# Performance work log

Hardware: AMD Instinct MI355X
Metric: run time of the kernel (lower is better)

Reference implementation:

```python
import jax, jax.numpy as jnp
import numpy as np

N_NODES = 100000
IN_DIM = 128
HIDDEN = 256
N_CLASSES = 16
N_EDGES = 1600000
N_GRAPHS = 64


def setup_inputs() -> dict:
    key = jax.random.key(0)
    ks = jax.random.split(key, 12)
    x = jax.random.normal(ks[0], (N_NODES, IN_DIM), dtype=jnp.float32)
    edge_index = jax.random.randint(ks[1], (2, N_EDGES), 0, N_NODES, dtype=jnp.int64)
    batch = jnp.sort(jax.random.randint(ks[2], (N_NODES,), 0, N_GRAPHS, dtype=jnp.int64))
    s = 0.05
    # SAGEConv layer 1: lin_l (on aggregated neighbors, with bias), lin_r (on root, no bias)
    W1l = jax.random.normal(ks[3], (IN_DIM, HIDDEN), dtype=jnp.float32) * s
    b1 = jnp.zeros((HIDDEN,), dtype=jnp.float32)
    W1r = jax.random.normal(ks[4], (IN_DIM, HIDDEN), dtype=jnp.float32) * s
    # SAGEConv layer 2
    W2l = jax.random.normal(ks[5], (HIDDEN, HIDDEN), dtype=jnp.float32) * s
    b2 = jnp.zeros((HIDDEN,), dtype=jnp.float32)
    W2r = jax.random.normal(ks[6], (HIDDEN, HIDDEN), dtype=jnp.float32) * s
    # final classifier
    fcW = jax.random.normal(ks[7], (HIDDEN, N_CLASSES), dtype=jnp.float32) * s
    fcb = jnp.zeros((N_CLASSES,), dtype=jnp.float32)
    return {"x": x, "edge_index": edge_index, "batch": batch,
            "W1l": W1l, "b1": b1, "W1r": W1r,
            "W2l": W2l, "b2": b2, "W2r": W2r,
            "fcW": fcW, "fcb": fcb}


def _sage_conv(x, src, dst, Wl, bl, Wr, n_nodes):
    # mean aggregation of neighbor features onto destination nodes
    agg = jax.ops.segment_sum(x[src], dst, num_segments=n_nodes)      # [N, d]
    deg = jax.ops.segment_sum(jnp.ones(src.shape, x.dtype), dst, num_segments=n_nodes)
    mean = agg / jnp.maximum(deg, 1.0)[:, None]
    # out = lin_l(mean_neighbors) + lin_r(x_root)  (PyG SAGEConv, mean aggr)
    return mean @ Wl + bl + x @ Wr


def reference(x, edge_index, batch, W1l, b1, W1r, W2l, b2, W2r, fcW, fcb):
    src, dst = edge_index[0], edge_index[1]
    h = jax.nn.relu(_sage_conv(x, src, dst, W1l, b1, W1r, N_NODES))
    # dropout is identity in inference mode
    h = jax.nn.relu(_sage_conv(h, src, dst, W2l, b2, W2r, N_NODES))
    # global mean pool over graphs in the batch
    g_sum = jax.ops.segment_sum(h, batch, num_segments=N_GRAPHS)      # [G, d]
    g_cnt = jax.ops.segment_sum(jnp.ones(batch.shape, h.dtype), batch, num_segments=N_GRAPHS)
    g = g_sum / jnp.maximum(g_cnt, 1.0)[:, None]
    return g @ fcW + fcb                                              # [G, num_classes]
```

## Files before the change

kernel.cpp:

```cpp
#include <hip/hip_runtime.h>

#define INDIM 128
#define HID 256
#define NCLS 16
#define NGRAPH 64
#define CHUNK 8192

typedef __bf16 bf16_t;
typedef bf16_t bf16x8 __attribute__((ext_vector_type(8)));
typedef float f32x4 __attribute__((ext_vector_type(4)));

__device__ __forceinline__ float bfu_lo(unsigned v) {
    union { unsigned i; float f; } u; u.i = v << 16; return u.f;
}
__device__ __forceinline__ float bfu_hi(unsigned v) {
    union { unsigned i; float f; } u; u.i = v & 0xffff0000u; return u.f;
}
__device__ __forceinline__ unsigned short f2bf(float f) {
    union { float f; unsigned i; } u; u.f = f;
    unsigned b = u.i;
    return (unsigned short)((b + 0x7fffu + ((b >> 16) & 1u)) >> 16);
}
__device__ __forceinline__ unsigned packbf(float lo, float hi) {
    return (unsigned)f2bf(lo) | ((unsigned)f2bf(hi) << 16);
}

typedef __attribute__((address_space(1))) const unsigned gu32_t;
typedef __attribute__((address_space(3))) unsigned lu32_t;
__device__ __forceinline__ void gl_lds16(const void* g, void* l) {
    __builtin_amdgcn_global_load_lds((gu32_t*)g, (lu32_t*)l, 16, 0, 0);
}

#define IACC(aE, aO, v)                              \
    do {                                             \
        aE[0] += ((v).x & 0x00FF00FFu);              \
        aO[0] += (((v).x >> 8) & 0x00FF00FFu);       \
        aE[1] += ((v).y & 0x00FF00FFu);              \
        aO[1] += (((v).y >> 8) & 0x00FF00FFu);       \
        aE[2] += ((v).z & 0x00FF00FFu);              \
        aO[2] += (((v).z >> 8) & 0x00FF00FFu);       \
        aE[3] += ((v).w & 0x00FF00FFu);              \
        aO[3] += (((v).w >> 8) & 0x00FF00FFu);       \
    } while (0)

__global__ void hist_kernel(const int* __restrict__ dst, int* __restrict__ deg, int E) {
    int e = blockIdx.x * blockDim.x + threadIdx.x;
    if (e < E) atomicAdd(&deg[dst[e]], 1);
}

__global__ void scan1_kernel(const int* __restrict__ deg, int* __restrict__ bsum, int n) {
    __shared__ int s[256];
    int t = threadIdx.x;
    int i = blockIdx.x * 256 + t;
    s[t] = (i < n) ? deg[i] : 0;
    __syncthreads();
    for (int off = 128; off > 0; off >>= 1) {
        if (t < off) s[t] += s[t + off];
        __syncthreads();
    }
    if (t == 0) bsum[blockIdx.x] = s[0];
}

__global__ void scan2_kernel(int* bsum, int nb) {
    __shared__ int s[1024];
    int t = threadIdx.x;
    int v = (t < nb) ? bsum[t] : 0;
    s[t] = v;
    __syncthreads();
    for (int off = 1; off < 1024; off <<= 1) {
        int u = (t >= off) ? s[t - off] : 0;
        __syncthreads();
        s[t] += u;
        __syncthreads();
    }
    if (t < nb) bsum[t] = s[t] - v;
}

__global__ void scan3_kernel(const int* __restrict__ deg, const int* __restrict__ bsum,
                             int* __restrict__ offs, int* __restrict__ gcur, int n) {
    __shared__ int s[256];
    int t = threadIdx.x;
    int i = blockIdx.x * 256 + t;
    int v = (i < n) ? deg[i] : 0;
    s[t] = v;
    __syncthreads();
    for (int off = 1; off < 256; off <<= 1) {
        int u = (t >= off) ? s[t - off] : 0;
        __syncthreads();
        s[t] += u;
        __syncthreads();
    }
    if (i < n) offs[i] = s[t] - v + bsum[blockIdx.x];
    if (t == 0) gcur[blockIdx.x] = bsum[blockIdx.x];
}

__global__ __launch_bounds__(256) void binA_kernel(const int* __restrict__ src,
                                                   const int* __restrict__ dst,
                                                   int* __restrict__ gcur,
                                                   unsigned* __restrict__ tmp,
                                                   int E, int nbuck) {
    __shared__ int hist[512];
    __shared__ int base[512];
    int t = threadIdx.x;
    int e0 = blockIdx.x * CHUNK;
    int e1 = min(e0 + CHUNK, E);
    for (int i = t; i < nbuck; i += 256) hist[i] = 0;
    __syncthreads();
    for (int e = e0 + t; e < e1; e += 256) atomicAdd(&hist[dst[e] >> 8], 1);
    __syncthreads();
    for (int i = t; i < nbuck; i += 256) {
        int c = hist[i];
        base[i] = (c > 0) ? atomicAdd(&gcur[i], c) : 0;
    }
    __syncthreads();
    for (int e = e0 + t; e < e1; e += 256) {
        int d = dst[e];
        int p = atomicAdd(&base[d >> 8], 1);
        tmp[p] = ((unsigned)(d & 255) << 17) | (unsigned)src[e];
    }
}

__global__ __launch_bounds__(256) void binB_kernel(const unsigned* __restrict__ tmp,
                                                   const int* __restrict__ offs,
                                                   int* __restrict__ srclist, int E, int n) {
    __shared__ int cur[256];
    int b = blockIdx.x;
    int node0 = b << 8;
    int nnodes = min(256, n - node0);
    int t = threadIdx.x;
    if (t < nnodes) cur[t] = offs[node0 + t];
    __syncthreads();
    int ebeg = offs[node0];
    int eend = (node0 + 256 < n) ? offs[node0 + 256] : E;
    for (int e = ebeg + t; e < eend; e += 256) {
        unsigned v = tmp[e];
        int p = atomicAdd(&cur[v >> 17], 1);
        srclist[p] = (int)(v & 0x1FFFFu);
    }
}

__global__ void prep_kernel(const float* __restrict__ x, unsigned short* __restrict__ xb,
                            const float* __restrict__ W1l, const float* __restrict__ W1r,
                            unsigned short* __restrict__ Bt1,
                            const float* __restrict__ W2l, const float* __restrict__ W2r,
                            unsigned short* __restrict__ Bt2, float* __restrict__ pmaxx,
                            int castb) {
    __shared__ float wmax[4];
    int b = blockIdx.x, t = threadIdx.x;
    if (b < castb) {
        int i4 = (b * 256 + t) * 4;
        float4 v = *(const float4*)(x + i4);
        *(ushort4*)(xb + i4) = make_ushort4(f2bf(v.x), f2bf(v.y), f2bf(v.z), f2bf(v.w));
        float m = fmaxf(fmaxf(fabsf(v.x), fabsf(v.y)), fmaxf(fabsf(v.z), fabsf(v.w)));
#pragma unroll
        for (int off = 32; off > 0; off >>= 1) m = fmaxf(m, __shfl_xor(m, off));
        if ((t & 63) == 0) wmax[t >> 6] = m;
        __syncthreads();
        if (t == 0)
            pmaxx[b] = fmaxf(fmaxf(wmax[0], wmax[1]), fmaxf(wmax[2], wmax[3]));
    } else if (b < castb + 256) {
        int idx = (b - castb) * 256 + t;
        int nn = idx >> 8, k = idx & 255;
        float v = (k < 128) ? W1l[(size_t)k * 256 + nn] : W1r[(size_t)(k - 128) * 256 + nn];
        Bt1[(size_t)nn * 256 + k] = f2bf(v);
    } else {
        int idx = (b - castb - 256) * 256 + t;
        int nn = idx >> 9, k = idx & 511;
        float v = (k < 256) ? W2l[(size_t)k * 256 + nn] : W2r[(size_t)(k - 256) * 256 + nn];
        Bt2[(size_t)nn * 512 + k] = f2bf(v);
    }
}

__global__ void reducemax_kernel(const float* __restrict__ pmax, int cnt,
                                 float* __restrict__ gmax) {
    __shared__ float wmax[4];
    int t = threadIdx.x;
    float m = 0.f;
    for (int i = t; i < cnt; i += 256) m = fmaxf(m, pmax[i]);
#pragma unroll
    for (int off = 32; off > 0; off >>= 1) m = fmaxf(m, __shfl_xor(m, off));
    if ((t & 63) == 0) wmax[t >> 6] = m;
    __syncthreads();
    if (t == 0) gmax[0] = fmaxf(fmaxf(wmax[0], wmax[1]), fmaxf(wmax[2], wmax[3]));
}

__global__ void cnt_kernel(const int* __restrict__ batch, float* __restrict__ cnt, int n) {
    __shared__ int h[64];
    int t = threadIdx.x;
    if (t < 64) h[t] = 0;
    __syncthreads();
    int i = blockIdx.x * 256 + t;
    if (i < n) atomicAdd(&h[batch[i]], 1);
    __syncthreads();
    if (t < 64 && h[t] > 0) atomicAdd(&cnt[t], (float)h[t]);
}

__global__ void quantx_kernel(const float* __restrict__ x, const float* __restrict__ gmaxp,
                              unsigned* __restrict__ xq, int total4) {
    int idx = blockIdx.x * blockDim.x + threadIdx.x;
    if (idx >= total4) return;
    float inv = 127.f / fmaxf(*gmaxp, 1e-20f);
    float4 v = *(const float4*)(x + idx * 4);
    int b0 = (int)fminf(fmaxf(rintf(v.x * inv), -127.f), 127.f) + 128;
    int b1 = (int)fminf(fmaxf(rintf(v.y * inv), -127.f), 127.f) + 128;
    int b2 = (int)fminf(fmaxf(rintf(v.z * inv), -127.f), 127.f) + 128;
    int b3 = (int)fminf(fmaxf(rintf(v.w * inv), -127.f), 127.f) + 128;
    xq[idx] = (unsigned)b0 | ((unsigned)b1 << 8) | ((unsigned)b2 << 16) | ((unsigned)b3 << 24);
}

__global__ void quanth_kernel(const unsigned short* __restrict__ h1, const float* __restrict__ gmaxp,
                              unsigned* __restrict__ hq, int total4) {
    int idx = blockIdx.x * blockDim.x + threadIdx.x;
    if (idx >= total4) return;
    float inv = 127.f / fmaxf(*gmaxp, 1e-20f);
    uint2 v = *(const uint2*)(h1 + idx * 4);
    int b0 = (int)fminf(rintf(bfu_lo(v.x) * inv), 127.f) + 128;
    int b1 = (int)fminf(rintf(bfu_hi(v.x) * inv), 127.f) + 128;
    int b2 = (int)fminf(rintf(bfu_lo(v.y) * inv), 127.f) + 128;
    int b3 = (int)fminf(rintf(bfu_hi(v.y) * inv), 127.f) + 128;
    hq[idx] = (unsigned)b0 | ((unsigned)b1 << 8) | ((unsigned)b2 << 16) | ((unsigned)b3 << 24);
}

__global__ void agg1_kernel(const unsigned char* __restrict__ xq, const int* __restrict__ srclist,
                            const int* __restrict__ offs, const int* __restrict__ deg,
                            const float* __restrict__ gmaxp,
                            unsigned short* __restrict__ mean, int n) {
    int gid = blockIdx.x * blockDim.x + threadIdx.x;
    int node = gid >> 6, lane = gid & 63;
    if (node >= n) return;
    int g = lane >> 3, sub = lane & 7;
    int st = __builtin_amdgcn_readfirstlane(offs[node]);
    int d = __builtin_amdgcn_readfirstlane(deg[node]);
    int end = st + d;
    unsigned aE[4] = {0, 0, 0, 0}, aO[4] = {0, 0, 0, 0};
    unsigned bE[4] = {0, 0, 0, 0}, bO[4] = {0, 0, 0, 0};
    const unsigned char* rb = xq + sub * 16;
    int e = st;
    for (; e + 15 < end; e += 16) {
        int s0 = srclist[e + g];
        int s1 = srclist[e + 8 + g];
        uint4 v0 = *(const uint4*)(rb + (size_t)s0 * 128);
        uint4 v1 = *(const uint4*)(rb + (size_t)s1 * 128);
        IACC(aE, aO, v0);
        IACC(bE, bO, v1);
    }
    for (; e + 7 < end; e += 8) {
        int s0 = srclist[e + g];
        uint4 v0 = *(const uint4*)(rb + (size_t)s0 * 128);
        IACC(aE, aO, v0);
    }
    int rem = end - e;
    if (rem > 0) {
        int s0 = srclist[e + ((g < rem) ? g : 0)];
        uint4 v0 = *(const uint4*)(rb + (size_t)s0 * 128);
        if (g < rem) IACC(aE, aO, v0);
    }
#pragma unroll
    for (int j = 0; j < 4; ++j) {
        unsigned se = aE[j] + bE[j], so = aO[j] + bO[j];
        se += (unsigned)__shfl_xor((int)se, 8);
        se += (unsigned)__shfl_xor((int)se, 16);
        se += (unsigned)__shfl_xor((int)se, 32);
        so += (unsigned)__shfl_xor((int)so, 8);
        so += (unsigned)__shfl_xor((int)so, 16);
        so += (unsigned)__shfl_xor((int)so, 32);
        aE[j] = se;
        aO[j] = so;
    }
    if (g == 0) {
        float sc = (*gmaxp) * (1.f / 127.f);
        float invd = 1.f / fmaxf((float)d, 1.f);
        unsigned o[8];
#pragma unroll
        for (int j = 0; j < 4; ++j) {
            float m0 = sc * (float)((int)(aE[j] & 0xFFFFu) - 128 * d) * invd;
            float m1 = sc * (float)((int)(aO[j] & 0xFFFFu) - 128 * d) * invd;
            float m2 = sc * (float)((int)(aE[j] >> 16) - 128 * d) * invd;
            float m3 = sc * (float)((int)(aO[j] >> 16) - 128 * d) * invd;
            o[j * 2] = packbf(m0, m1);
            o[j * 2 + 1] = packbf(m2, m3);
        }
        uint4* p = (uint4*)(mean + (size_t)node * 128 + sub * 16);
        p[0] = make_uint4(o[0], o[1], o[2], o[3]);
        p[1] = make_uint4(o[4], o[5], o[6], o[7]);
    }
}

__global__ void agg2_kernel(const unsigned char* __restrict__ hq, const int* __restrict__ srclist,
                            const int* __restrict__ offs, const int* __restrict__ deg,
                            const float* __restrict__ gmaxp,
                            unsigned short* __restrict__ mean, int n) {
    int gid = blockIdx.x * blockDim.x + threadIdx.x;
    int node = gid >> 6, lane = gid & 63;
    if (node >= n) return;
    int g = lane >> 4, sub = lane & 15;
    int st = __builtin_amdgcn_readfirstlane(offs[node]);
    int d = __builtin_amdgcn_readfirstlane(deg[node]);
    int end = st + d;
    unsigned aE[4] = {0, 0, 0, 0}, aO[4] = {0, 0, 0, 0};
    unsigned bE[4] = {0, 0, 0, 0}, bO[4] = {0, 0, 0, 0};
    const unsigned char* rb = hq + sub * 16;
    int e = st;
    for (; e + 7 < end; e += 8) {
        int s0 = srclist[e + g];
        int s1 = srclist[e + 4 + g];
        uint4 v0 = *(const uint4*)(rb + (size_t)s0 * 256);
        uint4 v1 = *(const uint4*)(rb + (size_t)s1 * 256);
        IACC(aE, aO, v0);
        IACC(bE, bO, v1);
    }
    for (; e + 3 < end; e += 4) {
        int s0 = srclist[e + g];
        uint4 v0 = *(const uint4*)(rb + (size_t)s0 * 256);
        IACC(aE, aO, v0);
    }
    int rem = end - e;
    if (rem > 0) {
        int s0 = srclist[e + ((g < rem) ? g : 0)];
        uint4 v0 = *(const uint4*)(rb + (size_t)s0 * 256);
        if (g < rem) IACC(aE, aO, v0);
    }
#pragma unroll
    for (int j = 0; j < 4; ++j) {
        unsigned se = aE[j] + bE[j], so = aO[j] + bO[j];
        se += (unsigned)__shfl_xor((int)se, 16);
        se += (unsigned)__shfl_xor((int)se, 32);
        so += (unsigned)__shfl_xor((int)so, 16);
        so += (unsigned)__shfl_xor((int)so, 32);
        aE[j] = se;
        aO[j] = so;
    }
    if (g == 0) {
        float sc = (*gmaxp) * (1.f / 127.f);
        float invd = 1.f / fmaxf((float)d, 1.f);
        unsigned o[8];
#pragma unroll
        for (int j = 0; j < 4; ++j) {
            float m0 = sc * (float)((int)(aE[j] & 0xFFFFu) - 128 * d) * invd;
            float m1 = sc * (float)((int)(aO[j] & 0xFFFFu) - 128 * d) * invd;
            float m2 = sc * (float)((int)(aE[j] >> 16) - 128 * d) * invd;
            float m3 = sc * (float)((int)(aO[j] >> 16) - 128 * d) * invd;
            o[j * 2] = packbf(m0, m1);
            o[j * 2 + 1] = packbf(m2, m3);
        }
        uint4* p = (uint4*)(mean + (size_t)node * 256 + sub * 16);
        p[0] = make_uint4(o[0], o[1], o[2], o[3]);
        p[1] = make_uint4(o[4], o[5], o[6], o[7]);
    }
}

template <int KH>
__global__ __launch_bounds__(256) void gemm_kernel(
        const bf16_t* __restrict__ A1, const bf16_t* __restrict__ A2,
        const bf16_t* __restrict__ Bt, const float* __restrict__ bias,
        unsigned short* __restrict__ H, float* __restrict__ pmax, int M) {
    constexpr int KT = 2 * KH;
    constexpr int NC = KT / 64;
    constexpr int CPH = KH / 64;
    __shared__ unsigned short As[64 * 64];
    __shared__ float wmax[4];
    int t = threadIdx.x, wave = t >> 6, lane = t & 63;
    int quad = lane >> 4, l16 = lane & 15;
    int row0 = blockIdx.x * 64, n0 = wave * 64;

    f32x4 acc[4][4];
#pragma unroll
    for (int i = 0; i < 4; ++i)
#pragma unroll
        for (int j = 0; j < 4; ++j) acc[i][j] = (f32x4)(0.f);

    int rA = wave * 8 + (lane >> 3);
    int kb = lane & 7;
    int kswA = (kb ^ (rA & 7)) << 3;
    unsigned short* ldsA = &As[(size_t)(wave * 8) * 64];
    unsigned short* ldsB = &As[(size_t)(32 + wave * 8) * 64];

    const bf16_t* Bp = Bt + (size_t)(n0 + l16) * KT + quad * 8;

    for (int c = 0; c < NC; ++c) {
        const bf16_t* Ah = (c < CPH) ? A1 : A2;
        int kk = ((c < CPH) ? c : (c - CPH)) * 64;
        gl_lds16(Ah + (size_t)(row0 + rA) * KH + kk + kswA, ldsA);
        gl_lds16(Ah + (size_t)(row0 + 32 + rA) * KH + kk + kswA, ldsB);
        __syncthreads();
        int bk = c * 64;
#pragma unroll
        for (int sub = 0; sub < 2; ++sub) {
            bf16x8 af[4], bfr[4];
#pragma unroll
            for (int mi = 0; mi < 4; ++mi) {
                int r = mi * 16 + l16;
                int qb = sub * 4 + quad;
                af[mi] = *(const bf16x8*)&As[r * 64 + ((qb ^ (r & 7)) << 3)];
            }
#pragma unroll
            for (int ni = 0; ni < 4; ++ni)
                bfr[ni] = *(const bf16x8*)(Bp + (size_t)(ni * 16) * KT + bk + sub * 32);
#pragma unroll
            for (int mi = 0; mi < 4; ++mi)
#pragma unroll
                for (int ni = 0; ni < 4; ++ni)
                    acc[mi][ni] = __builtin_amdgcn_mfma_f32_16x16x32_bf16(
                        af[mi], bfr[ni], acc[mi][ni], 0, 0, 0);
        }
        __syncthreads();
    }

    float bv[4];
#pragma unroll
    for (int ni = 0; ni < 4; ++ni) bv[ni] = bias[n0 + ni * 16 + l16];
    float mloc = 0.f;
#pragma unroll
    for (int mi = 0; mi < 4; ++mi) {
#pragma unroll
        for (int r = 0; r < 4; ++r) {
            int row = row0 + mi * 16 + quad * 4 + r;
            if (row < M) {
#pragma unroll
                for (int ni = 0; ni < 4; ++ni) {
                    int col = n0 + ni * 16 + l16;
                    float hv = fmaxf(acc[mi][ni][r] + bv[ni], 0.f);
                    mloc = fmaxf(mloc, hv);
                    H[(size_t)row * 256 + col] = f2bf(hv);
                }
            }
        }
    }
    if (pmax) {
#pragma unroll
        for (int off = 32; off > 0; off >>= 1) mloc = fmaxf(mloc, __shfl_xor(mloc, off));
        if (lane == 0) wmax[wave] = mloc;
        __syncthreads();
        if (t == 0)
            pmax[blockIdx.x] = fmaxf(fmaxf(wmax[0], wmax[1]), fmaxf(wmax[2], wmax[3]));
    }
}

__global__ __launch_bounds__(256) void gemm2p_kernel(
        const bf16_t* __restrict__ A1, const bf16_t* __restrict__ A2,
        const bf16_t* __restrict__ Bt, const float* __restrict__ bias,
        const int* __restrict__ batch, float* __restrict__ g, int M) {
    constexpr int KH = 256, KT = 512, NC = 8, CPH = 4;
    __shared__ unsigned short As[64 * 64];
    __shared__ int sbatch[64];
    int t = threadIdx.x, wave = t >> 6, lane = t & 63;
    int quad = lane >> 4, l16 = lane & 15;
    int row0 = blockIdx.x * 64, n0 = wave * 64;

    if (t < 64) sbatch[t] = (row0 + t < M) ? batch[row0 + t] : -1;

    f32x4 acc[4][4];
#pragma unroll
    for (int i = 0; i < 4; ++i)
#pragma unroll
        for (int j = 0; j < 4; ++j) acc[i][j] = (f32x4)(0.f);

    int rA = wave * 8 + (lane >> 3);
    int kb = lane & 7;
    int kswA = (kb ^ (rA & 7)) << 3;
    unsigned short* ldsA = &As[(size_t)(wave * 8) * 64];
    unsigned short* ldsB = &As[(size_t)(32 + wave * 8) * 64];

    const bf16_t* Bp = Bt + (size_t)(n0 + l16) * KT + quad * 8;

    for (int c = 0; c < NC; ++c) {
        const bf16_t* Ah = (c < CPH) ? A1 : A2;
        int kk = ((c < CPH) ? c : (c - CPH)) * 64;
        gl_lds16(Ah + (size_t)(row0 + rA) * KH + kk + kswA, ldsA);
        gl_lds16(Ah + (size_t)(row0 + 32 + rA) * KH + kk + kswA, ldsB);
        __syncthreads();
        int bk = c * 64;
#pragma unroll
        for (int sub = 0; sub < 2; ++sub) {
            bf16x8 af[4], bfr[4];
#pragma unroll
            for (int mi = 0; mi < 4; ++mi) {
                int r = mi * 16 + l16;
                int qb = sub * 4 + quad;
                af[mi] = *(const bf16x8*)&As[r * 64 + ((qb ^ (r & 7)) << 3)];
            }
#pragma unroll
            for (int ni = 0; ni < 4; ++ni)
                bfr[ni] = *(const bf16x8*)(Bp + (size_t)(ni * 16) * KT + bk + sub * 32);
#pragma unroll
            for (int mi = 0; mi < 4; ++mi)
#pragma unroll
                for (int ni = 0; ni < 4; ++ni)
                    acc[mi][ni] = __builtin_amdgcn_mfma_f32_16x16x32_bf16(
                        af[mi], bfr[ni], acc[mi][ni], 0, 0, 0);
        }
        __syncthreads();
    }

    float bv[4];
#pragma unroll
    for (int ni = 0; ni < 4; ++ni) bv[ni] = bias[n0 + ni * 16 + l16];

    int rlast = min(63, M - 1 - row0);
    int b0 = sbatch[0], b1 = sbatch[rlast];
    for (int gb = b0; gb <= b1; ++gb) {
        float colsum[4] = {0.f, 0.f, 0.f, 0.f};
#pragma unroll
        for (int mi = 0; mi < 4; ++mi) {
#pragma unroll
            for (int r = 0; r < 4; ++r) {
                int rl = mi * 16 + quad * 4 + r;
                if (sbatch[rl] == gb) {
#pragma unroll
                    for (int ni = 0; ni < 4; ++ni)
                        colsum[ni] += fmaxf(acc[mi][ni][r] + bv[ni], 0.f);
                }
            }
        }
#pragma unroll
        for (int ni = 0; ni < 4; ++ni) {
            colsum[ni] += __shfl_xor(colsum[ni], 16);
            colsum[ni] += __shfl_xor(colsum[ni], 32);
        }
        if (lane < 16) {
#pragma unroll
            for (int ni = 0; ni < 4; ++ni)
                atomicAdd(&g[gb * 256 + n0 + ni * 16 + l16], colsum[ni]);
        }
    }
}

__global__ void final_kernel(const float* __restrict__ g, const float* __restrict__ cnt,
                             const float* __restrict__ fcW, const float* __restrict__ fcb,
                             float* __restrict__ out) {
    int t = threadIdx.x;
    for (int o = t; o < NGRAPH * NCLS; o += 256) {
        int gi = o >> 4, c = o & 15;
        float inv = 1.f / fmaxf(cnt[gi], 1.f);
        float dot = 0.f;
        for (int k = 0; k < 256; ++k) dot += g[gi * 256 + k] * fcW[k * 16 + c];
        out[o] = dot * inv + fcb[c];
    }
}

extern "C" void kernel_launch(void* const* d_in, const int* in_sizes, int n_in, void* d_out,
                              int out_size, void* d_ws, size_t ws_size, hipStream_t stream) {
    const float* x   = (const float*)d_in[0];
    const int* edge  = (const int*)d_in[1];
    const int* batch = (const int*)d_in[2];
    const float* W1l = (const float*)d_in[3];
    const float* b1  = (const float*)d_in[4];
    const float* W1r = (const float*)d_in[5];
    const float* W2l = (const float*)d_in[6];
    const float* b2  = (const float*)d_in[7];
    const float* W2r = (const float*)d_in[8];
    const float* fcW = (const float*)d_in[9];
    const float* fcb = (const float*)d_in[10];
    float* out = (float*)d_out;

    const int n = in_sizes[0] / INDIM;
    const int E = in_sizes[1] / 2;
    const int* src = edge;
    const int* dst = edge + E;
    const int nbuck = (n + 255) >> 8;

    char* ws = (char*)d_ws;
    size_t off = 0;
    auto alloc = [&](size_t bytes) {
        size_t p = off;
        off = (off + bytes + 511) & ~(size_t)511;
        return p;
    };
    size_t offs_o    = alloc((size_t)n * 4);
    size_t deg_o     = alloc((size_t)n * 4);
    size_t cnt_o     = alloc(64 * 4);
    size_t g_o       = alloc(64 * 256 * 4);
    size_t gmax_o    = alloc(8);
    size_t zero_end  = off;
    size_t pmax_o    = alloc(12544 * 4);
    size_t bsum_o    = alloc(1024 * 4);
    size_t gcur_o    = alloc(512 * 4);
    size_t srclist_o = alloc((size_t)E * 4);
    size_t bt1_o     = alloc(256 * 256 * 2);
    size_t bt2_o     = alloc(256 * 512 * 2);
    size_t xbm2_o    = alloc((size_t)n * 256 * 2);
    size_t mean1_o   = alloc((size_t)n * 128 * 2);
    size_t h1_o      = alloc((size_t)n * 256 * 2);
    size_t aux_o     = alloc((size_t)n * 256 * 2);

    int*   offs    = (int*)(ws + offs_o);
    int*   deg     = (int*)(ws + deg_o);
    float* cnt     = (float*)(ws + cnt_o);
    float* g       = (float*)(ws + g_o);
    float* gmaxx   = (float*)(ws + gmax_o);
    float* gmaxh   = (float*)(ws + gmax_o + 4);
    float* pmax    = (float*)(ws + pmax_o);
    int*   bsum    = (int*)(ws + bsum_o);
    int*   gcur    = (int*)(ws + gcur_o);
    int*   srclist = (int*)(ws + srclist_o);
    unsigned short* Bt1   = (unsigned short*)(ws + bt1_o);
    unsigned short* Bt2   = (unsigned short*)(ws + bt2_o);
    unsigned short* xb16  = (unsigned short*)(ws + xbm2_o);
    unsigned char*  xq8   = (unsigned char*)(ws + xbm2_o + (size_t)n * 256);
    unsigned short* mean2 = (unsigned short*)(ws + xbm2_o);
    unsigned short* mean1 = (unsigned short*)(ws + mean1_o);
    unsigned short* h1b   = (unsigned short*)(ws + h1_o);
    unsigned*       tmp   = (unsigned*)(ws + aux_o);
    unsigned char*  hq8   = (unsigned char*)(ws + aux_o + (size_t)n * 256);

    hipMemsetAsync(ws + deg_o, 0, zero_end - deg_o, stream);

    int eb = (E + 255) / 256;
    int nb = (n + 255) / 256;
    hist_kernel<<<eb, 256, 0, stream>>>(dst, deg, E);
    scan1_kernel<<<nb, 256, 0, stream>>>(deg, bsum, n);
    scan2_kernel<<<1, 1024, 0, stream>>>(bsum, nb);
    scan3_kernel<<<nb, 256, 0, stream>>>(deg, bsum, offs, gcur, n);
    binA_kernel<<<(E + CHUNK - 1) / CHUNK, 256, 0, stream>>>(src, dst, gcur, tmp, E, nbuck);
    binB_kernel<<<nbuck, 256, 0, stream>>>(tmp, offs, srclist, E, n);

    int castb = n * INDIM / 4 / 256;
    prep_kernel<<<castb + 256 + 512, 256, 0, stream>>>(x, xb16, W1l, W1r, Bt1, W2l, W2r, Bt2,
                                                       pmax, castb);
    reducemax_kernel<<<1, 256, 0, stream>>>(pmax, castb, gmaxx);
    cnt_kernel<<<nb, 256, 0, stream>>>(batch, cnt, n);
    int xq4 = n * INDIM / 4;
    quantx_kernel<<<(xq4 + 255) / 256, 256, 0, stream>>>(x, gmaxx, (unsigned*)xq8, xq4);

    int aggb = (n * 64 + 255) / 256;
    int gemmb = (n + 63) / 64;

    agg1_kernel<<<aggb, 256, 0, stream>>>(xq8, srclist, offs, deg, gmaxx, mean1, n);
    gemm_kernel<128><<<gemmb, 256, 0, stream>>>(
        (const bf16_t*)mean1, (const bf16_t*)xb16, (const bf16_t*)Bt1, b1, h1b, pmax, n);
    reducemax_kernel<<<1, 256, 0, stream>>>(pmax, gemmb, gmaxh);
    int hq4 = n * HID / 4;
    quanth_kernel<<<(hq4 + 255) / 256, 256, 0, stream>>>(h1b, gmaxh, (unsigned*)hq8, hq4);
    agg2_kernel<<<aggb, 256, 0, stream>>>(hq8, srclist, offs, deg, gmaxh, mean2, n);
    gemm2p_kernel<<<gemmb, 256, 0, stream>>>(
        (const bf16_t*)mean2, (const bf16_t*)h1b, (const bf16_t*)Bt2, b2, batch, g, n);

    final_kernel<<<1, 256, 0, stream>>>(g, cnt, fcW, fcb, out);
}
```

Measured before the change: 536.4 us.

## Halve GEMM row tile to 32 and double-buffer A tiles in LDS

Both node GEMM kernels now use a 32-row tile instead of 64, which doubles the block count, and they double-buffer the A tile in shared memory. The next K chunk is prefetched while MFMAs run on the current one, leaving one barrier per iteration instead of two. The intent is to hide global-to-LDS load latency and raise occupancy. In exchange, each B fragment read from global/L2 feeds only half as many MFMAs, so B traffic per output row roughly doubles.

```diff
diff --git a/kernel.cpp b/kernel.cpp
--- a/kernel.cpp
+++ b/kernel.cpp
@@ -357,53 +357,56 @@
     constexpr int KT = 2 * KH;
     constexpr int NC = KT / 64;
     constexpr int CPH = KH / 64;
-    __shared__ unsigned short As[64 * 64];
+    __shared__ unsigned short As[2][32 * 64];
     __shared__ float wmax[4];
     int t = threadIdx.x, wave = t >> 6, lane = t & 63;
     int quad = lane >> 4, l16 = lane & 15;
-    int row0 = blockIdx.x * 64, n0 = wave * 64;
-
-    f32x4 acc[4][4];
-#pragma unroll
-    for (int i = 0; i < 4; ++i)
+    int row0 = blockIdx.x * 32, n0 = wave * 64;
+
+    f32x4 acc[2][4];
+#pragma unroll
+    for (int i = 0; i < 2; ++i)
 #pragma unroll
         for (int j = 0; j < 4; ++j) acc[i][j] = (f32x4)(0.f);
 
     int rA = wave * 8 + (lane >> 3);
     int kb = lane & 7;
-    int kswA = (kb ^ (rA & 7)) << 3;
-    unsigned short* ldsA = &As[(size_t)(wave * 8) * 64];
-    unsigned short* ldsB = &As[(size_t)(32 + wave * 8) * 64];
-
+    int ksw = (kb ^ (rA & 7)) << 3;
     const bf16_t* Bp = Bt + (size_t)(n0 + l16) * KT + quad * 8;
 
+    {
+        const bf16_t* Ah = (0 < CPH) ? A1 : A2;
+        gl_lds16(Ah + (size_t)(row0 + rA) * KH + ksw, &As[0][(wave * 8) * 64]);
+    }
     for (int c = 0; c < NC; ++c) {
-        const bf16_t* Ah = (c < CPH) ? A1 : A2;
-        int kk = ((c < CPH) ? c : (c - CPH)) * 64;
-        gl_lds16(Ah + (size_t)(row0 + rA) * KH + kk + kswA, ldsA);
-        gl_lds16(Ah + (size_t)(row0 + 32 + rA) * KH + kk + kswA, ldsB);
-        __syncthreads();
+        __syncthreads();
+        if (c + 1 < NC) {
+            int cn = c + 1;
+            const bf16_t* Ah = (cn < CPH) ? A1 : A2;
+            int kk = ((cn < CPH) ? cn : cn - CPH) * 64;
+            gl_lds16(Ah + (size_t)(row0 + rA) * KH + kk + ksw, &As[cn & 1][(wave * 8) * 64]);
+        }
+        const unsigned short* Ab = As[c & 1];
         int bk = c * 64;
 #pragma unroll
         for (int sub = 0; sub < 2; ++sub) {
-            bf16x8 af[4], bfr[4];
-#pragma unroll
-            for (int mi = 0; mi < 4; ++mi) {
+            bf16x8 af[2], bfr[4];
+#pragma unroll
+            for (int mi = 0; mi < 2; ++mi) {
                 int r = mi * 16 + l16;
                 int qb = sub * 4 + quad;
-                af[mi] = *(const bf16x8*)&As[r * 64 + ((qb ^ (r & 7)) << 3)];
+                af[mi] = *(const bf16x8*)&Ab[r * 64 + ((qb ^ (r & 7)) << 3)];
             }
 #pragma unroll
             for (int ni = 0; ni < 4; ++ni)
                 bfr[ni] = *(const bf16x8*)(Bp + (size_t)(ni * 16) * KT + bk + sub * 32);
 #pragma unroll
-            for (int mi = 0; mi < 4; ++mi)
+            for (int mi = 0; mi < 2; ++mi)
 #pragma unroll
                 for (int ni = 0; ni < 4; ++ni)
                     acc[mi][ni] = __builtin_amdgcn_mfma_f32_16x16x32_bf16(
                         af[mi], bfr[ni], acc[mi][ni], 0, 0, 0);
         }
-        __syncthreads();
     }
 
     float bv[4];
@@ -411,7 +414,7 @@
     for (int ni = 0; ni < 4; ++ni) bv[ni] = bias[n0 + ni * 16 + l16];
     float mloc = 0.f;
 #pragma unroll
-    for (int mi = 0; mi < 4; ++mi) {
+    for (int mi = 0; mi < 2; ++mi) {
 #pragma unroll
         for (int r = 0; r < 4; ++r) {
             int row = row0 + mi * 16 + quad * 4 + r;
@@ -441,67 +444,67 @@
         const bf16_t* __restrict__ Bt, const float* __restrict__ bias,
         const int* __restrict__ batch, float* __restrict__ g, int M) {
     constexpr int KH = 256, KT = 512, NC = 8, CPH = 4;
-    __shared__ unsigned short As[64 * 64];
-    __shared__ int sbatch[64];
+    __shared__ unsigned short As[2][32 * 64];
+    __shared__ int sbatch[32];
     int t = threadIdx.x, wave = t >> 6, lane = t & 63;
     int quad = lane >> 4, l16 = lane & 15;
-    int row0 = blockIdx.x * 64, n0 = wave * 64;
-
-    if (t < 64) sbatch[t] = (row0 + t < M) ? batch[row0 + t] : -1;
-
-    f32x4 acc[4][4];
-#pragma unroll
-    for (int i = 0; i < 4; ++i)
+    int row0 = blockIdx.x * 32, n0 = wave * 64;
+
+    if (t < 32) sbatch[t] = (row0 + t < M) ? batch[row0 + t] : -1;
+
+    f32x4 acc[2][4];
+#pragma unroll
+    for (int i = 0; i < 2; ++i)
 #pragma unroll
         for (int j = 0; j < 4; ++j) acc[i][j] = (f32x4)(0.f);
 
     int rA = wave * 8 + (lane >> 3);
     int kb = lane & 7;
-    int kswA = (kb ^ (rA & 7)) << 3;
-    unsigned short* ldsA = &As[(size_t)(wave * 8) * 64];
-    unsigned short* ldsB = &As[(size_t)(32 + wave * 8) * 64];
-
+    int ksw = (kb ^ (rA & 7)) << 3;
     const bf16_t* Bp = Bt + (size_t)(n0 + l16) * KT + quad * 8;
 
+    gl_lds16(A1 + (size_t)(row0 + rA) * KH + ksw, &As[0][(wave * 8) * 64]);
     for (int c = 0; c < NC; ++c) {
-        const bf16_t* Ah = (c < CPH) ? A1 : A2;
-        int kk = ((c < CPH) ? c : (c - CPH)) * 64;
-        gl_lds16(Ah + (size_t)(row0 + rA) * KH + kk + kswA, ldsA);
-        gl_lds16(Ah + (size_t)(row0 + 32 + rA) * KH + kk + kswA, ldsB);
-        __syncthreads();
+        __syncthreads();
+        if (c + 1 < NC) {
+            int cn = c + 1;
+            const bf16_t* Ah = (cn < CPH) ? A1 : A2;
+            int kk = ((cn < CPH) ? cn : cn - CPH) * 64;
+            gl_lds16(Ah + (size_t)(row0 + rA) * KH + kk + ksw, &As[cn & 1][(wave * 8) * 64]);
+        }
+        const unsigned short* Ab = As[c & 1];
         int bk = c * 64;
 #pragma unroll
         for (int sub = 0; sub < 2; ++sub) {
-            bf16x8 af[4], bfr[4];
-#pragma unroll
-            for (int mi = 0; mi < 4; ++mi) {
+            bf16x8 af[2], bfr[4];
+#pragma unroll
+            for (int mi = 0; mi < 2; ++mi) {
                 int r = mi * 16 + l16;
                 int qb = sub * 4 + quad;
-                af[mi] = *(const bf16x8*)&As[r * 64 + ((qb ^ (r & 7)) << 3)];
+                af[mi] = *(const bf16x8*)&Ab[r * 64 + ((qb ^ (r & 7)) << 3)];
             }
 #pragma unroll
             for (int ni = 0; ni < 4; ++ni)
                 bfr[ni] = *(const bf16x8*)(Bp + (size_t)(ni * 16) * KT + bk + sub * 32);
 #pragma unroll
-            for (int mi = 0; mi < 4; ++mi)
+            for (int mi = 0; mi < 2; ++mi)
 #pragma unroll
                 for (int ni = 0; ni < 4; ++ni)
                     acc[mi][ni] = __builtin_amdgcn_mfma_f32_16x16x32_bf16(
                         af[mi], bfr[ni], acc[mi][ni], 0, 0, 0);
         }
-        __syncthreads();
     }
 
     float bv[4];
 #pragma unroll
     for (int ni = 0; ni < 4; ++ni) bv[ni] = bias[n0 + ni * 16 + l16];
 
-    int rlast = min(63, M - 1 - row0);
+    int rlast = min(31, M - 1 - row0);
     int b0 = sbatch[0], b1 = sbatch[rlast];
     for (int gb = b0; gb <= b1; ++gb) {
         float colsum[4] = {0.f, 0.f, 0.f, 0.f};
 #pragma unroll
-        for (int mi = 0; mi < 4; ++mi) {
+        for (int mi = 0; mi < 2; ++mi) {
 #pragma unroll
             for (int r = 0; r < 4; ++r) {
                 int rl = mi * 16 + quad * 4 + r;
@@ -623,7 +626,7 @@
     quantx_kernel<<<(xq4 + 255) / 256, 256, 0, stream>>>(x, gmaxx, (unsigned*)xq8, xq4);
 
     int aggb = (n * 64 + 255) / 256;
-    int gemmb = (n + 63) / 64;
+    int gemmb = (n + 31) / 32;
 
     agg1_kernel<<<aggb, 256, 0, stream>>>(xq8, srclist, offs, deg, gmaxx, mean1, n);
     gemm_kernel<128><<<gemmb, 256, 0, stream>>>(
```

After: 576.5 us. +7.5%, slower.
